# Kernel optimization log

Measured on AMD Instinct MI355X. Metric: run time of the kernel, lower is better.

Reference implementation:

```python
import jax, jax.numpy as jnp
import numpy as np

B, L, C = 4, 1024, 768
H = 12
D = C // H  # head_dim = 64


def setup_inputs() -> dict:
    key = jax.random.key(0)
    k_x, k_qkv, k_pw, k_pb = jax.random.split(key, 4)
    x = jax.random.normal(k_x, (B, L, C), dtype=jnp.float32)
    # torch nn.Linear(C, 3C, bias=False): weight [3C, C]
    w_qkv = jax.random.normal(k_qkv, (3 * C, C), dtype=jnp.float32) * (1.0 / np.sqrt(C))
    # torch nn.Linear(C, C): weight [C, C], bias [C]
    w_proj = jax.random.normal(k_pw, (C, C), dtype=jnp.float32) * (1.0 / np.sqrt(C))
    b_proj = jax.random.normal(k_pb, (C,), dtype=jnp.float32) * 0.01
    return {"x": x, "w_qkv": w_qkv, "w_proj": w_proj, "b_proj": b_proj}


def reference(x, w_qkv, w_proj, b_proj):
    scale = D ** (-0.5)
    # qkv: [B, L, 3C] -> [3, B, H, L, D]
    qkv = jnp.einsum('blc,fc->blf', x, w_qkv)
    qkv = qkv.reshape(B, L, 3, H, D).transpose(2, 0, 3, 1, 4)
    q, k, v = qkv[0], qkv[1], qkv[2]
    # attention scores [B, H, L, L], materialized (returned by the module)
    attn = jnp.einsum('bhld,bhmd->bhlm', q, k) * scale
    attn_score = jax.nn.softmax(attn, axis=-1)
    # dropout_p = 0.0 -> identity
    out = jnp.einsum('bhlm,bhmd->bhld', attn_score, v)
    out = out.transpose(0, 2, 1, 3).reshape(B, L, C)
    out = jnp.einsum('blc,fc->blf', out, w_proj) + b_proj
    return (out, attn_score)
```

## Files before the change

kernel.cpp:

```cpp
#include <hip/hip_runtime.h>
#include <hip/hip_bf16.h>
#include <stdint.h>


typedef __attribute__((ext_vector_type(8))) short short8;
typedef __attribute__((ext_vector_type(4))) float floatx4;

#define MFMA16(A_, B_, C_) __builtin_amdgcn_mfma_f32_16x16x32_bf16((A_), (B_), (C_), 0, 0, 0)

__device__ __forceinline__ unsigned short f2bf(float f) {
  unsigned u = __builtin_bit_cast(unsigned, f);
  u += 0x7FFFu + ((u >> 16) & 1u);
  return (unsigned short)(u >> 16);
}
__device__ __forceinline__ float bf2f(unsigned short u) {
  return __builtin_bit_cast(float, (unsigned)u << 16);
}

__global__ __launch_bounds__(256) void cast3_kernel(const float* __restrict__ x,
                                                    const float* __restrict__ wq,
                                                    const float* __restrict__ wp,
                                                    unsigned short* __restrict__ dst) {
  const int NX = 3145728, NWQ = 1769472;
  int i = (blockIdx.x * 256 + threadIdx.x) * 4;
  const float* src;
  int off;
  if (i < NX) { src = x; off = i; }
  else if (i < NX + NWQ) { src = wq; off = i - NX; }
  else { src = wp; off = i - NX - NWQ; }
  float4 v = *(const float4*)(src + off);
  ushort4 o;
  o.x = f2bf(v.x); o.y = f2bf(v.y); o.z = f2bf(v.z); o.w = f2bf(v.w);
  *(ushort4*)(dst + i) = o;
}

template <int EPI, int BN>
__global__ __launch_bounds__(256) void gemm_bt(
    const unsigned short* __restrict__ A, const unsigned short* __restrict__ Bm,
    const float* __restrict__ bias,
    unsigned short* __restrict__ q_ws, unsigned short* __restrict__ k_ws,
    unsigned short* __restrict__ vt_ws, float* __restrict__ Cout,
    int M, int N, int K) {
  constexpr int NJ = BN / 32;
  constexpr int QN = BN / 2;
  __shared__ __align__(16) unsigned short Al[2][128 * 32];
  __shared__ __align__(16) unsigned short Bl[2][BN * 32];
  const int tid = threadIdx.x;
  const int lane = tid & 63, wave = tid >> 6;
  const int q = lane >> 4, lm = lane & 15;
  const int wm = wave >> 1, wn = wave & 1;
  const int m0 = blockIdx.y * 128, n0 = blockIdx.x * BN;

  floatx4 acc[4][NJ];
#pragma unroll
  for (int i = 0; i < 4; ++i)
#pragma unroll
    for (int j = 0; j < NJ; ++j) acc[i][j] = (floatx4){0.f, 0.f, 0.f, 0.f};

  auto stage = [&](int k0, int buf) {
#pragma unroll
    for (int it = 0; it < 2; ++it) {
      int idx = tid + it * 256;
      int row = idx >> 2, ch = idx & 3;
      const unsigned short* ga = A + (size_t)(m0 + row) * K + k0 + ch * 8;
      __builtin_amdgcn_global_load_lds(
          (const __attribute__((address_space(1))) unsigned int*)ga,
          (__attribute__((address_space(3))) unsigned int*)(&Al[buf][0] + idx * 8), 16, 0, 0);
    }
#pragma unroll
    for (int it = 0; it < BN / 64; ++it) {
      int idx = tid + it * 256;
      int row = idx >> 2, ch = idx & 3;
      const unsigned short* gb = Bm + (size_t)(n0 + row) * K + k0 + ch * 8;
      __builtin_amdgcn_global_load_lds(
          (const __attribute__((address_space(1))) unsigned int*)gb,
          (__attribute__((address_space(3))) unsigned int*)(&Bl[buf][0] + idx * 8), 16, 0, 0);
    }
  };

  stage(0, 0);
  __syncthreads();
  int cur = 0;
  for (int k0 = 0; k0 < K; k0 += 32) {
    if (k0 + 32 < K) stage(k0 + 32, cur ^ 1);
    short8 af[4], bfr[NJ];
#pragma unroll
    for (int t = 0; t < 4; ++t)
      af[t] = *(const short8*)(&Al[cur][0] + (wm * 64 + t * 16 + lm) * 32 + q * 8);
#pragma unroll
    for (int t = 0; t < NJ; ++t)
      bfr[t] = *(const short8*)(&Bl[cur][0] + (wn * QN + t * 16 + lm) * 32 + q * 8);
#pragma unroll
    for (int i = 0; i < 4; ++i)
#pragma unroll
      for (int j = 0; j < NJ; ++j) acc[i][j] = MFMA16(af[i], bfr[j], acc[i][j]);
    __syncthreads();
    cur ^= 1;
  }

  if (EPI == 0) {
#pragma unroll
    for (int i = 0; i < 4; ++i) {
      int mb = m0 + wm * 64 + i * 16 + q * 4;
#pragma unroll
      for (int j = 0; j < NJ; ++j) {
        int n = n0 + wn * QN + j * 16 + lm;
        int which = n / 768;
        int r = n - which * 768;
        int h = r >> 6, d = r & 63;
        if (which == 2) {
          int b = mb >> 10, l = mb & 1023;
          ushort4 pk;
          pk.x = f2bf(acc[i][j][0]);
          pk.y = f2bf(acc[i][j][1]);
          pk.z = f2bf(acc[i][j][2]);
          pk.w = f2bf(acc[i][j][3]);
          *(ushort4*)(vt_ws + (size_t)((b * 12 + h) * 64 + d) * 1024 + l) = pk;
        } else {
          unsigned short* dst = (which == 0) ? q_ws : k_ws;
          float sc = (which == 0) ? 0.125f : 1.0f;
#pragma unroll
          for (int rg = 0; rg < 4; ++rg) {
            int m = mb + rg;
            int b = m >> 10, l = m & 1023;
            dst[(size_t)((b * 12 + h) * 1024 + l) * 64 + d] = f2bf(acc[i][j][rg] * sc);
          }
        }
      }
    }
  } else {
#pragma unroll
    for (int i = 0; i < 4; ++i) {
      int mb = m0 + wm * 64 + i * 16 + q * 4;
#pragma unroll
      for (int j = 0; j < NJ; ++j) {
        int n = n0 + wn * QN + j * 16 + lm;
        float bv = bias[n];
#pragma unroll
        for (int rg = 0; rg < 4; ++rg) {
          int m = mb + rg;
          Cout[(size_t)m * N + n] = acc[i][j][rg] + bv;
        }
      }
    }
  }
}

__global__ __launch_bounds__(256) void attn_mfma(
    const unsigned short* __restrict__ q_ws, const unsigned short* __restrict__ k_ws,
    const unsigned short* __restrict__ vt_ws, unsigned short* __restrict__ attn_o,
    float* __restrict__ out1) {
  constexpr int L = 1024, SW = 1032;
  __shared__ __align__(16) unsigned short S[16 * SW];
  __shared__ float stats[2][4][16];
  const int bh = blockIdx.y, b = bh / 12, h = bh % 12;
  const int l0 = blockIdx.x * 16;
  const int tid = threadIdx.x, lane = tid & 63, wave = tid >> 6;
  const int q = lane >> 4, lm = lane & 15;

  const size_t qk_base = (size_t)bh * L * 64;

  const unsigned short* qr = q_ws + qk_base + (size_t)(l0 + lm) * 64;
  short8 bq0 = *(const short8*)(qr + q * 8);
  short8 bq1 = *(const short8*)(qr + 32 + q * 8);

  floatx4 acc[16];
#pragma unroll
  for (int ct = 0; ct < 16; ++ct) {
    const unsigned short* kr = k_ws + qk_base + (size_t)((wave * 16 + ct) * 16 + lm) * 64;
    short8 a0 = *(const short8*)(kr + q * 8);
    short8 a1 = *(const short8*)(kr + 32 + q * 8);
    floatx4 c = (floatx4){0.f, 0.f, 0.f, 0.f};
    c = MFMA16(a0, bq0, c);
    c = MFMA16(a1, bq1, c);
    acc[ct] = c;
  }

  float mloc = -1e30f;
#pragma unroll
  for (int ct = 0; ct < 16; ++ct)
#pragma unroll
    for (int rg = 0; rg < 4; ++rg) mloc = fmaxf(mloc, acc[ct][rg]);
  mloc = fmaxf(mloc, __shfl_xor(mloc, 16));
  mloc = fmaxf(mloc, __shfl_xor(mloc, 32));
  if (lane < 16) stats[0][wave][lane] = mloc;
  __syncthreads();
  float m = fmaxf(fmaxf(stats[0][0][lm], stats[0][1][lm]),
                  fmaxf(stats[0][2][lm], stats[0][3][lm]));

  float ssum = 0.f;
#pragma unroll
  for (int ct = 0; ct < 16; ++ct) {
#pragma unroll
    for (int rg = 0; rg < 4; ++rg) {
      float e = exp2f((acc[ct][rg] - m) * 1.44269504f);
      acc[ct][rg] = e;
      ssum += e;
    }
  }
  ssum += __shfl_xor(ssum, 16);
  ssum += __shfl_xor(ssum, 32);
  if (lane < 16) stats[1][wave][lane] = ssum;
  __syncthreads();
  float sinv = 1.0f / (stats[1][0][lm] + stats[1][1][lm] + stats[1][2][lm] + stats[1][3][lm]);

  float* orow = out1 + (size_t)bh * L * L + (size_t)(l0 + lm) * L + wave * 256 + q * 4;
  unsigned short* srow = S + lm * SW + wave * 256 + q * 4;
#pragma unroll
  for (int ct = 0; ct < 16; ++ct) {
    float p0 = acc[ct][0] * sinv, p1 = acc[ct][1] * sinv;
    float p2 = acc[ct][2] * sinv, p3 = acc[ct][3] * sinv;
    ushort4 pk;
    pk.x = f2bf(p0); pk.y = f2bf(p1); pk.z = f2bf(p2); pk.w = f2bf(p3);
    *(ushort4*)(srow + ct * 16) = pk;
    float4 pv;
    pv.x = p0; pv.y = p1; pv.z = p2; pv.w = p3;
    *(float4*)(orow + ct * 16) = pv;
  }
  __syncthreads();

  {
    floatx4 pacc = (floatx4){0.f, 0.f, 0.f, 0.f};
    const unsigned short* vr = vt_ws + (size_t)(bh * 64 + wave * 16 + lm) * 1024;
#pragma unroll 4
    for (int ks = 0; ks < 32; ++ks) {
      short8 af = *(const short8*)(S + lm * SW + ks * 32 + q * 8);
      short8 bv = *(const short8*)(vr + ks * 32 + q * 8);
      pacc = MFMA16(af, bv, pacc);
    }
#pragma unroll
    for (int rg = 0; rg < 4; ++rg) {
      int row = q * 4 + rg;
      attn_o[(size_t)(b * 1024 + l0 + row) * 768 + h * 64 + wave * 16 + lm] = f2bf(pacc[rg]);
    }
  }
}

extern "C" void kernel_launch(void* const* d_in, const int* in_sizes, int n_in,
                              void* d_out, int out_size, void* d_ws, size_t ws_size,
                              hipStream_t stream) {
  const float* x      = (const float*)d_in[0];
  const float* w_qkv  = (const float*)d_in[1];
  const float* w_proj = (const float*)d_in[2];
  const float* b_proj = (const float*)d_in[3];

  float* out0 = (float*)d_out;
  float* out1 = out0 + (size_t)4096 * 768;

  const size_t NX = (size_t)4096 * 768;
  const size_t NWQ = (size_t)2304 * 768;
  const size_t NWP = (size_t)768 * 768;
  const size_t NQ = (size_t)48 * 1024 * 64;

  unsigned short* x_bf   = (unsigned short*)d_ws;
  unsigned short* wq_bf  = x_bf + NX;
  unsigned short* wp_bf  = wq_bf + NWQ;
  unsigned short* q_ws   = wp_bf + NWP;
  unsigned short* k_ws   = q_ws + NQ;
  unsigned short* vt_ws  = k_ws + NQ;
  unsigned short* attn_o = vt_ws + NQ;

  cast3_kernel<<<dim3((NX + NWQ + NWP) / 1024), dim3(256), 0, stream>>>(x, w_qkv, w_proj, x_bf);

  gemm_bt<0, 128><<<dim3(2304 / 128, 4096 / 128), dim3(256), 0, stream>>>(
      x_bf, wq_bf, nullptr, q_ws, k_ws, vt_ws, nullptr, 4096, 2304, 768);

  attn_mfma<<<dim3(64, 48), dim3(256), 0, stream>>>(q_ws, k_ws, vt_ws, attn_o, out1);

  gemm_bt<1, 64><<<dim3(768 / 64, 4096 / 128), dim3(256), 0, stream>>>(
      attn_o, wp_bf, b_proj, nullptr, nullptr, nullptr, out0, 4096, 768, 768);
}
```

Measured before the change: 357.2 us.

## Merge softmax barriers with per-wave rescaling, swizzle grid for XCDs, add setprio

Each wave now exponentiates against its own local max, and the per-wave max and sum are exchanged through a single barrier, with a rescale factor applied afterwards. This removes one of the two block-wide syncs in the softmax. The grid is flattened to 1D and swizzled so consecutive blocks on the same XCD share a (batch, head) for better K/V L2 reuse. s_setprio is raised around the MFMA loops. Numerics shift slightly because the bf16 values and the sums are computed relative to per-wave maxima.

```diff
diff --git a/kernel.cpp b/kernel.cpp
--- a/kernel.cpp
+++ b/kernel.cpp
@@ -151,10 +151,13 @@
     const unsigned short* __restrict__ vt_ws, unsigned short* __restrict__ attn_o,
     float* __restrict__ out1) {
   constexpr int L = 1024, SW = 1032;
+  constexpr float LOG2E = 1.44269504f;
   __shared__ __align__(16) unsigned short S[16 * SW];
   __shared__ float stats[2][4][16];
-  const int bh = blockIdx.y, b = bh / 12, h = bh % 12;
-  const int l0 = blockIdx.x * 16;
+  const int flat = blockIdx.x;
+  const int swz = (flat & 7) * 384 + (flat >> 3);
+  const int bh = swz >> 6, b = bh / 12, h = bh % 12;
+  const int l0 = (swz & 63) * 16;
   const int tid = threadIdx.x, lane = tid & 63, wave = tid >> 6;
   const int q = lane >> 4, lm = lane & 15;
 
@@ -165,6 +168,7 @@
   short8 bq1 = *(const short8*)(qr + 32 + q * 8);
 
   floatx4 acc[16];
+  __builtin_amdgcn_s_setprio(1);
 #pragma unroll
   for (int ct = 0; ct < 16; ++ct) {
     const unsigned short* kr = k_ws + qk_base + (size_t)((wave * 16 + ct) * 16 + lm) * 64;
@@ -175,6 +179,7 @@
     c = MFMA16(a1, bq1, c);
     acc[ct] = c;
   }
+  __builtin_amdgcn_s_setprio(0);
 
   float mloc = -1e30f;
 #pragma unroll
@@ -183,33 +188,40 @@
     for (int rg = 0; rg < 4; ++rg) mloc = fmaxf(mloc, acc[ct][rg]);
   mloc = fmaxf(mloc, __shfl_xor(mloc, 16));
   mloc = fmaxf(mloc, __shfl_xor(mloc, 32));
-  if (lane < 16) stats[0][wave][lane] = mloc;
-  __syncthreads();
-  float m = fmaxf(fmaxf(stats[0][0][lm], stats[0][1][lm]),
-                  fmaxf(stats[0][2][lm], stats[0][3][lm]));
 
   float ssum = 0.f;
 #pragma unroll
   for (int ct = 0; ct < 16; ++ct) {
 #pragma unroll
     for (int rg = 0; rg < 4; ++rg) {
-      float e = exp2f((acc[ct][rg] - m) * 1.44269504f);
+      float e = exp2f((acc[ct][rg] - mloc) * LOG2E);
       acc[ct][rg] = e;
       ssum += e;
     }
   }
   ssum += __shfl_xor(ssum, 16);
   ssum += __shfl_xor(ssum, 32);
-  if (lane < 16) stats[1][wave][lane] = ssum;
+  if (lane < 16) {
+    stats[0][wave][lane] = mloc;
+    stats[1][wave][lane] = ssum;
+  }
   __syncthreads();
-  float sinv = 1.0f / (stats[1][0][lm] + stats[1][1][lm] + stats[1][2][lm] + stats[1][3][lm]);
+
+  float m0_ = stats[0][0][lm], m1_ = stats[0][1][lm];
+  float m2_ = stats[0][2][lm], m3_ = stats[0][3][lm];
+  float m = fmaxf(fmaxf(m0_, m1_), fmaxf(m2_, m3_));
+  float sum = stats[1][0][lm] * exp2f((m0_ - m) * LOG2E)
+            + stats[1][1][lm] * exp2f((m1_ - m) * LOG2E)
+            + stats[1][2][lm] * exp2f((m2_ - m) * LOG2E)
+            + stats[1][3][lm] * exp2f((m3_ - m) * LOG2E);
+  float wscale = exp2f((mloc - m) * LOG2E) / sum;
 
   float* orow = out1 + (size_t)bh * L * L + (size_t)(l0 + lm) * L + wave * 256 + q * 4;
   unsigned short* srow = S + lm * SW + wave * 256 + q * 4;
 #pragma unroll
   for (int ct = 0; ct < 16; ++ct) {
-    float p0 = acc[ct][0] * sinv, p1 = acc[ct][1] * sinv;
-    float p2 = acc[ct][2] * sinv, p3 = acc[ct][3] * sinv;
+    float p0 = acc[ct][0] * wscale, p1 = acc[ct][1] * wscale;
+    float p2 = acc[ct][2] * wscale, p3 = acc[ct][3] * wscale;
     ushort4 pk;
     pk.x = f2bf(p0); pk.y = f2bf(p1); pk.z = f2bf(p2); pk.w = f2bf(p3);
     *(ushort4*)(srow + ct * 16) = pk;
@@ -222,12 +234,14 @@
   {
     floatx4 pacc = (floatx4){0.f, 0.f, 0.f, 0.f};
     const unsigned short* vr = vt_ws + (size_t)(bh * 64 + wave * 16 + lm) * 1024;
+    __builtin_amdgcn_s_setprio(1);
 #pragma unroll 4
     for (int ks = 0; ks < 32; ++ks) {
       short8 af = *(const short8*)(S + lm * SW + ks * 32 + q * 8);
       short8 bv = *(const short8*)(vr + ks * 32 + q * 8);
       pacc = MFMA16(af, bv, pacc);
     }
+    __builtin_amdgcn_s_setprio(0);
 #pragma unroll
     for (int rg = 0; rg < 4; ++rg) {
       int row = q * 4 + rg;
@@ -265,7 +279,7 @@
   gemm_bt<0, 128><<<dim3(2304 / 128, 4096 / 128), dim3(256), 0, stream>>>(
       x_bf, wq_bf, nullptr, q_ws, k_ws, vt_ws, nullptr, 4096, 2304, 768);
 
-  attn_mfma<<<dim3(64, 48), dim3(256), 0, stream>>>(q_ws, k_ws, vt_ws, attn_o, out1);
+  attn_mfma<<<dim3(3072), dim3(256), 0, stream>>>(q_ws, k_ws, vt_ws, attn_o, out1);
 
   gemm_bt<1, 64><<<dim3(768 / 64, 4096 / 128), dim3(256), 0, stream>>>(
       attn_o, wp_bf, b_proj, nullptr, nullptr, nullptr, out0, 4096, 768, 768);
```

New measurement: 339.0 us. 5.1% less time.
